# Kernel optimization log

Measured on AMD Instinct MI355X. Metric: run time of the kernel, lower is better.

Reference implementation:

```python
import jax, jax.numpy as jnp
import numpy as np

N_EDGES = 4096
HIDDEN = 256
EDGE_DIM = 128
NUM_HEADS = 4
NUM_GRAPHS = 64


def setup_inputs() -> dict:
    key0 = jax.random.key(0)
    ks = jax.random.split(key0, 10)
    s = 0.02
    inp = {
        "query": jax.random.normal(ks[0], (N_EDGES, HIDDEN), jnp.float32),
        "key": jax.random.normal(ks[1], (N_EDGES, EDGE_DIM), jnp.float32),
        "value": jax.random.normal(ks[2], (N_EDGES, EDGE_DIM), jnp.float32),
        "edge_graph_index": jnp.sort(
            jax.random.randint(ks[3], (N_EDGES,), 0, NUM_GRAPHS)
        ),
        # edge_proj: Linear(edge_context_dim -> hidden_dim)
        "w_edge": jax.random.normal(ks[4], (HIDDEN, EDGE_DIM), jnp.float32) * s,
        "b_edge": jnp.zeros((HIDDEN,), jnp.float32),
        # nn.MultiheadAttention packed in-projection [3H, H] and bias [3H]
        "w_in": jax.random.normal(ks[5], (3 * HIDDEN, HIDDEN), jnp.float32) * s,
        "b_in": jnp.zeros((3 * HIDDEN,), jnp.float32),
        # out_proj: Linear(hidden -> hidden)
        "w_out": jax.random.normal(ks[6], (HIDDEN, HIDDEN), jnp.float32) * s,
        "b_out": jnp.zeros((HIDDEN,), jnp.float32),
    }
    return inp


def reference(query, key, value, edge_graph_index,
              w_edge, b_edge, w_in, b_in, w_out, b_out):
    # Segment-wise cross attention == block-diagonal masked attention over all edges.
    N, H = query.shape
    nh = NUM_HEADS
    dh = H // nh

    # edge feature projection (applied to both key and value, as in the module)
    K = key @ w_edge.T + b_edge      # [N, H]
    V = value @ w_edge.T + b_edge    # [N, H]

    wq, wk, wv = jnp.split(w_in, 3, axis=0)
    bq, bk, bv = jnp.split(b_in, 3)
    Qh = (query @ wq.T + bq).reshape(N, nh, dh)
    Kh = (K @ wk.T + bk).reshape(N, nh, dh)
    Vh = (V @ wv.T + bv).reshape(N, nh, dh)

    scale = 1.0 / jnp.sqrt(jnp.asarray(dh, query.dtype))
    scores = jnp.einsum("nhd,mhd->hnm", Qh, Kh) * scale  # [nh, N, N]

    # attention only within the same graph segment
    same_graph = edge_graph_index[:, None] == edge_graph_index[None, :]  # [N, N]
    neg = jnp.finfo(scores.dtype).min
    scores = jnp.where(same_graph[None, :, :], scores, neg)

    attn = jax.nn.softmax(scores, axis=-1)                 # [nh, N, N]
    out = jnp.einsum("hnm,mhd->nhd", attn, Vh).reshape(N, H)
    out = out @ w_out.T + b_out
    return query + out
```

## Files before the change

kernel.cpp:

```cpp
#include <hip/hip_runtime.h>

#define N_EDGES 4096
#define HIDDEN  256
#define EDGE_DIM 128
#define NUM_HEADS 4
#define NUM_GRAPHS 64
#define DH 64

typedef __attribute__((ext_vector_type(8))) short short8;
typedef __attribute__((ext_vector_type(4))) float f32x4;

__device__ __forceinline__ unsigned short f2bf(float f) {
  unsigned u = __builtin_bit_cast(unsigned, f);
  u += 0x7FFF + ((u >> 16) & 1);
  return (unsigned short)(u >> 16);
}
__device__ __forceinline__ float bf2f(unsigned short u) {
  return __builtin_bit_cast(float, (unsigned)u << 16);
}
__device__ __forceinline__ short8 cvt8(float4 x, float4 y) {
  short8 v;
  v[0] = (short)f2bf(x.x); v[1] = (short)f2bf(x.y);
  v[2] = (short)f2bf(x.z); v[3] = (short)f2bf(x.w);
  v[4] = (short)f2bf(y.x); v[5] = (short)f2bf(y.y);
  v[6] = (short)f2bf(y.z); v[7] = (short)f2bf(y.w);
  return v;
}
__device__ __forceinline__ float4 us4f(ushort4 v) {
  float4 f;
  f.x = bf2f(v.x); f.y = bf2f(v.y); f.z = bf2f(v.z); f.w = bf2f(v.w);
  return f;
}

__device__ __forceinline__ int lbound(const int* __restrict__ a, int n, int v) {
  int lo = 0, hi = n;
  while (lo < hi) { int mid = (lo + hi) >> 1; if (a[mid] < v) lo = mid + 1; else hi = mid; }
  return lo;
}

template<bool ABF, bool WBF, bool OUTF32>
__device__ __forceinline__ void gemm_tile(const void* Ap, const void* Wp,
                                          const float* __restrict__ bias,
                                          const float* __restrict__ res,
                                          void* Cp, const int K,
                                          const int m0, const int n0,
                                          unsigned short* As, unsigned short* Ws) {
  const int t = threadIdx.x;
  const int r = t >> 2, kg = t & 3;
  const int lane = t & 63, w = t >> 6;
  const int quad = lane >> 4, l16 = lane & 15;
  const int wm = (w >> 1) * 32, wn = (w & 1) * 32;
  f32x4 acc[2][2] = {};
  const float*          pa32 = (const float*)Ap          + (size_t)(m0 + r) * K + kg * 16;
  const unsigned short* pa16 = (const unsigned short*)Ap + (size_t)(m0 + r) * K + kg * 16;
  const float*          pw32 = (const float*)Wp          + (size_t)(n0 + r) * K + kg * 16;
  const unsigned short* pw16 = (const unsigned short*)Wp + (size_t)(n0 + r) * K + kg * 16;
  float4 a0, a1, a2, a3, w0, w1, w2, w3;
  short8 a16a, a16b, w16a, w16b;
  if (ABF) { a16a = *(const short8*)pa16; a16b = *(const short8*)(pa16 + 8); }
  else { a0 = *(const float4*)pa32;       a1 = *(const float4*)(pa32 + 4);
         a2 = *(const float4*)(pa32 + 8); a3 = *(const float4*)(pa32 + 12); }
  if (WBF) { w16a = *(const short8*)pw16; w16b = *(const short8*)(pw16 + 8); }
  else { w0 = *(const float4*)pw32;       w1 = *(const float4*)(pw32 + 4);
         w2 = *(const float4*)(pw32 + 8); w3 = *(const float4*)(pw32 + 12); }
  for (int kc = 0; kc < K; kc += 64) {
    short8 na16a, na16b, nw16a, nw16b;
    float4 na0, na1, na2, na3, nw0, nw1, nw2, nw3;
    if (kc + 64 < K) {
      if (ABF) { na16a = *(const short8*)(pa16 + kc + 64);
                 na16b = *(const short8*)(pa16 + kc + 72); }
      else { na0 = *(const float4*)(pa32 + kc + 64); na1 = *(const float4*)(pa32 + kc + 68);
             na2 = *(const float4*)(pa32 + kc + 72); na3 = *(const float4*)(pa32 + kc + 76); }
      if (WBF) { nw16a = *(const short8*)(pw16 + kc + 64);
                 nw16b = *(const short8*)(pw16 + kc + 72); }
      else { nw0 = *(const float4*)(pw32 + kc + 64); nw1 = *(const float4*)(pw32 + kc + 68);
             nw2 = *(const float4*)(pw32 + kc + 72); nw3 = *(const float4*)(pw32 + kc + 76); }
    }
    __syncthreads();
    *(short8*)&As[r * 72 + kg * 16]     = ABF ? a16a : cvt8(a0, a1);
    *(short8*)&As[r * 72 + kg * 16 + 8] = ABF ? a16b : cvt8(a2, a3);
    *(short8*)&Ws[r * 72 + kg * 16]     = WBF ? w16a : cvt8(w0, w1);
    *(short8*)&Ws[r * 72 + kg * 16 + 8] = WBF ? w16b : cvt8(w2, w3);
    __syncthreads();
#pragma unroll
    for (int ks = 0; ks < 2; ++ks) {
      short8 af0 = *(const short8*)&As[(wm + l16) * 72 + ks * 32 + quad * 8];
      short8 af1 = *(const short8*)&As[(wm + 16 + l16) * 72 + ks * 32 + quad * 8];
      short8 bq0 = *(const short8*)&Ws[(wn + l16) * 72 + ks * 32 + quad * 8];
      short8 bq1 = *(const short8*)&Ws[(wn + 16 + l16) * 72 + ks * 32 + quad * 8];
      acc[0][0] = __builtin_amdgcn_mfma_f32_16x16x32_bf16(af0, bq0, acc[0][0], 0, 0, 0);
      acc[0][1] = __builtin_amdgcn_mfma_f32_16x16x32_bf16(af0, bq1, acc[0][1], 0, 0, 0);
      acc[1][0] = __builtin_amdgcn_mfma_f32_16x16x32_bf16(af1, bq0, acc[1][0], 0, 0, 0);
      acc[1][1] = __builtin_amdgcn_mfma_f32_16x16x32_bf16(af1, bq1, acc[1][1], 0, 0, 0);
    }
    a16a = na16a; a16b = na16b; a0 = na0; a1 = na1; a2 = na2; a3 = na3;
    w16a = nw16a; w16b = nw16b; w0 = nw0; w1 = nw1; w2 = nw2; w3 = nw3;
  }
#pragma unroll
  for (int j = 0; j < 2; ++j) {
    const int col = n0 + wn + j * 16 + l16;
    const float bj = bias[col];
#pragma unroll
    for (int i = 0; i < 2; ++i)
#pragma unroll
      for (int reg = 0; reg < 4; ++reg) {
        const int row = m0 + wm + i * 16 + quad * 4 + reg;
        const size_t idx = (size_t)row * HIDDEN + col;
        float v = acc[i][j][reg] + bj;
        if (OUTF32) ((float*)Cp)[idx] = v + res[idx];
        else        ((unsigned short*)Cp)[idx] = f2bf(v);
      }
  }
}

__device__ __forceinline__ void wf_part(int bb, const float* __restrict__ w_in,
                                        const float* __restrict__ b_in,
                                        const float* __restrict__ w_edge,
                                        const float* __restrict__ b_edge,
                                        unsigned short* __restrict__ Wfk,
                                        unsigned short* __restrict__ Wfv,
                                        float* __restrict__ bfk, float* __restrict__ bfv,
                                        unsigned short* As, unsigned short* Bs) {
  const int sel = bb >> 3;
  const int tt  = bb & 7;
  const int n0  = (tt >> 1) * 64;
  const int k0  = (tt & 1) * 64;
  const float* Wp = w_in + (size_t)(256 + 256 * sel) * HIDDEN;
  const float* bp = b_in + 256 + 256 * sel;
  unsigned short* Wf = sel ? Wfv : Wfk;
  float* bf = sel ? bfv : bfk;
  const int t = threadIdx.x;
  const int r = t >> 2, kg = t & 3;
  const int lane = t & 63, w = t >> 6;
  const int quad = lane >> 4, l16 = lane & 15;
  const int wm = (w >> 1) * 32, wn = (w & 1) * 32;
  if (k0 == 0) {
    float s = 0.f;
    const float* wrow = Wp + (size_t)(n0 + r) * HIDDEN + kg * 64;
    const float* be = b_edge + kg * 64;
#pragma unroll
    for (int j = 0; j < 64; j += 4) {
      float4 a = *(const float4*)(wrow + j);
      float4 b = *(const float4*)(be + j);
      s += a.x * b.x + a.y * b.y + a.z * b.z + a.w * b.w;
    }
    s += __shfl_xor(s, 1); s += __shfl_xor(s, 2);
    if (kg == 0) bf[n0 + r] = s + bp[n0 + r];
  }
  f32x4 facc[2][2] = {};
  for (int j0 = 0; j0 < HIDDEN; j0 += 32) {
    __syncthreads();
    { const float* p = Wp + (size_t)(n0 + r) * HIDDEN + j0 + kg * 8;
      float4 x0 = *(const float4*)p, x1 = *(const float4*)(p + 4);
      *(short8*)&As[r * 40 + kg * 8] = cvt8(x0, x1); }
    { const int j = t >> 3, k8 = (t & 7) * 8;
      const float* p = w_edge + (size_t)(j0 + j) * EDGE_DIM + k0 + k8;
      float4 b0 = *(const float4*)p, b1 = *(const float4*)(p + 4);
      float bv[8] = {b0.x, b0.y, b0.z, b0.w, b1.x, b1.y, b1.z, b1.w};
#pragma unroll
      for (int i = 0; i < 8; ++i) Bs[(k8 + i) * 40 + j] = f2bf(bv[i]); }
    __syncthreads();
    short8 af0 = *(const short8*)&As[(wm + l16) * 40 + quad * 8];
    short8 af1 = *(const short8*)&As[(wm + 16 + l16) * 40 + quad * 8];
    short8 bq0 = *(const short8*)&Bs[(wn + l16) * 40 + quad * 8];
    short8 bq1 = *(const short8*)&Bs[(wn + 16 + l16) * 40 + quad * 8];
    facc[0][0] = __builtin_amdgcn_mfma_f32_16x16x32_bf16(af0, bq0, facc[0][0], 0, 0, 0);
    facc[0][1] = __builtin_amdgcn_mfma_f32_16x16x32_bf16(af0, bq1, facc[0][1], 0, 0, 0);
    facc[1][0] = __builtin_amdgcn_mfma_f32_16x16x32_bf16(af1, bq0, facc[1][0], 0, 0, 0);
    facc[1][1] = __builtin_amdgcn_mfma_f32_16x16x32_bf16(af1, bq1, facc[1][1], 0, 0, 0);
  }
#pragma unroll
  for (int jj = 0; jj < 2; ++jj)
#pragma unroll
    for (int ii = 0; ii < 2; ++ii)
#pragma unroll
      for (int reg = 0; reg < 4; ++reg) {
        const int n = wm + ii * 16 + quad * 4 + reg;
        const int k = wn + jj * 16 + l16;
        Wf[(size_t)(n0 + n) * EDGE_DIM + k0 + k] = f2bf(facc[ii][jj][reg]);
      }
}

__global__ __launch_bounds__(256) void k_wf(const float* __restrict__ w_in,
                                            const float* __restrict__ b_in,
                                            const float* __restrict__ w_edge,
                                            const float* __restrict__ b_edge,
                                            const int* __restrict__ gidx,
                                            unsigned short* Wfk, unsigned short* Wfv,
                                            float* bfk, float* bfv, int* segStart) {
  __shared__ unsigned short As[64 * 40];
  __shared__ unsigned short Bs[64 * 40];
  if (blockIdx.x < 16)
    wf_part(blockIdx.x, w_in, b_in, w_edge, b_edge, Wfk, Wfv, bfk, bfv, As, Bs);
  else if (threadIdx.x <= NUM_GRAPHS)
    segStart[threadIdx.x] = lbound(gidx, N_EDGES, threadIdx.x);
}

__global__ __launch_bounds__(256) void k_proj(const float* __restrict__ query,
                                              const float* __restrict__ key,
                                              const float* __restrict__ value,
                                              const float* __restrict__ w_in,
                                              const float* __restrict__ b_in,
                                              const unsigned short* __restrict__ Wfk,
                                              const unsigned short* __restrict__ Wfv,
                                              const float* __restrict__ bfk,
                                              const float* __restrict__ bfv,
                                              unsigned short* Qh, unsigned short* Kh,
                                              unsigned short* Vh) {
  __shared__ unsigned short As[64 * 72];
  __shared__ unsigned short Ws[64 * 72];
  const int m0 = blockIdx.x * 64, n0 = blockIdx.y * 64;
  if (blockIdx.z == 0)
    gemm_tile<false, false, false>(query, w_in, b_in, nullptr, Qh, 256, m0, n0, As, Ws);
  else if (blockIdx.z == 1)
    gemm_tile<false, true, false>(key, Wfk, bfk, nullptr, Kh, 128, m0, n0, As, Ws);
  else
    gemm_tile<false, true, false>(value, Wfv, bfv, nullptr, Vh, 128, m0, n0, As, Ws);
}

__global__ __launch_bounds__(256) void attn_segment(const unsigned short* __restrict__ Qh,
                                                    const unsigned short* __restrict__ Kh,
                                                    const unsigned short* __restrict__ Vh,
                                                    const int* __restrict__ segStart,
                                                    unsigned short* __restrict__ ao) {
  const int graph = blockIdx.x, h = blockIdx.y, zg = blockIdx.z;
  const int segLo = segStart[graph];
  const int segHi = segStart[graph + 1];
  const int segLen = segHi - segLo;
  const int t = threadIdx.x, lane = t & 63, w = t >> 6;
  __shared__ float Qs[16][68], Ks[64][68], Vs[64][68];
  __shared__ float Ps[4][64][4];
  const float scale = 0.125f;
  const int r0 = w * 4;

  for (int chunk = zg; chunk * 16 < segLen; chunk += 8) {
    const int row0 = segLo + chunk * 16;
    const int rows = min(16, segHi - row0);
    __syncthreads();
    { int r = t >> 4, d4 = (t & 15) * 4;
      if (r < rows)
        *(float4*)&Qs[r][d4] =
            us4f(*(const ushort4*)(Qh + (size_t)(row0 + r) * HIDDEN + h * DH + d4)); }

    float accv[4] = {0.f, 0.f, 0.f, 0.f}, lsum[4] = {0.f, 0.f, 0.f, 0.f};

    for (int c0 = segLo; c0 < segHi; c0 += 64) {
      const int tc = min(64, segHi - c0);
      __syncthreads();
#pragma unroll
      for (int it = 0; it < 4; ++it) {
        int s = t + it * 256; int j = s >> 4; int d4 = (s & 15) * 4;
        if (j < tc) {
          *(float4*)&Ks[j][d4] =
              us4f(*(const ushort4*)(Kh + (size_t)(c0 + j) * HIDDEN + h * DH + d4));
          *(float4*)&Vs[j][d4] =
              us4f(*(const ushort4*)(Vh + (size_t)(c0 + j) * HIDDEN + h * DH + d4));
        }
      }
      __syncthreads();
      float4 kreg[16];
#pragma unroll
      for (int d4 = 0; d4 < 16; ++d4) kreg[d4] = *(const float4*)&Ks[lane][d4 * 4];
      float p[4];
#pragma unroll
      for (int r = 0; r < 4; ++r) {
        float s = 0.f;
#pragma unroll
        for (int d4 = 0; d4 < 16; ++d4) {
          float4 q = *(const float4*)&Qs[r0 + r][d4 * 4];
          s += q.x * kreg[d4].x + q.y * kreg[d4].y + q.z * kreg[d4].z + q.w * kreg[d4].w;
        }
        p[r] = (lane < tc && r0 + r < rows) ? __expf(s * scale) : 0.f;
        lsum[r] += p[r];
      }
      float4 p4; p4.x = p[0]; p4.y = p[1]; p4.z = p[2]; p4.w = p[3];
      *(float4*)&Ps[w][lane][0] = p4;
      __asm__ volatile("s_waitcnt lgkmcnt(0)" ::: "memory");
      for (int j = 0; j < tc; ++j) {
        const float v = Vs[j][lane];
        float4 pj = *(const float4*)&Ps[w][j][0];
        accv[0] += pj.x * v; accv[1] += pj.y * v;
        accv[2] += pj.z * v; accv[3] += pj.w * v;
      }
    }
#pragma unroll
    for (int off = 32; off; off >>= 1)
#pragma unroll
      for (int r = 0; r < 4; ++r) lsum[r] += __shfl_xor(lsum[r], off);
#pragma unroll
    for (int r = 0; r < 4; ++r)
      if (r0 + r < rows)
        ao[(size_t)(row0 + r0 + r) * HIDDEN + h * DH + lane] = f2bf(accv[r] / lsum[r]);
  }
}

__global__ __launch_bounds__(256) void k_out(const unsigned short* __restrict__ ao,
                                             const float* __restrict__ w_out,
                                             const float* __restrict__ b_out,
                                             const float* __restrict__ query,
                                             float* __restrict__ out) {
  __shared__ unsigned short As[64 * 72];
  __shared__ unsigned short Ws[64 * 72];
  gemm_tile<true, false, true>(ao, w_out, b_out, query, out, 256,
                               blockIdx.x * 64, blockIdx.y * 64, As, Ws);
}

extern "C" void kernel_launch(void* const* d_in, const int* in_sizes, int n_in,
                              void* d_out, int out_size, void* d_ws, size_t ws_size,
                              hipStream_t stream) {
  const float* query  = (const float*)d_in[0];
  const float* key    = (const float*)d_in[1];
  const float* value  = (const float*)d_in[2];
  const int*   gidx   = (const int*)d_in[3];
  const float* w_edge = (const float*)d_in[4];
  const float* b_edge = (const float*)d_in[5];
  const float* w_in   = (const float*)d_in[6];
  const float* b_in   = (const float*)d_in[7];
  const float* w_out  = (const float*)d_in[8];
  const float* b_out  = (const float*)d_in[9];
  float* out = (float*)d_out;

  int* segStart = (int*)d_ws;
  unsigned short* Qh  = (unsigned short*)((char*)d_ws + 512);
  unsigned short* Kh  = Qh + (size_t)N_EDGES * HIDDEN;
  unsigned short* Vh  = Kh + (size_t)N_EDGES * HIDDEN;
  unsigned short* ao  = Vh + (size_t)N_EDGES * HIDDEN;
  unsigned short* Wfk = ao + (size_t)N_EDGES * HIDDEN;
  unsigned short* Wfv = Wfk + 256 * EDGE_DIM;
  float* bfk = (float*)(Wfv + 256 * EDGE_DIM);
  float* bfv = bfk + 256;

  k_wf<<<dim3(17), 256, 0, stream>>>(w_in, b_in, w_edge, b_edge, gidx,
                                     Wfk, Wfv, bfk, bfv, segStart);
  k_proj<<<dim3(64, 4, 3), 256, 0, stream>>>(query, key, value, w_in, b_in,
                                             Wfk, Wfv, bfk, bfv, Qh, Kh, Vh);
  attn_segment<<<dim3(NUM_GRAPHS, NUM_HEADS, 8), 256, 0, stream>>>(Qh, Kh, Vh,
                                                                   segStart, ao);
  k_out<<<dim3(64, 4), 256, 0, stream>>>(ao, w_out, b_out, query, out);
}
```

Measured before the change: 121.3 us.

## Fuse edge projection and K/V in-projection into single QKV kernel

Removes the separate weight-folding kernel and merges the K/V projection with the edge projection. Each K/V block first computes the edge-projected 64x256 tile into LDS, then multiplies it by the in-projection weights, and Q tiles plus the segment-boundary search run in the same launch. This saves one kernel launch and the dependency between the fold and projection kernels. In exchange, K/V blocks do a two-stage GEMM with more FLOPs per row, use a larger LDS footprint (which may lower occupancy), and get only 128 heavy blocks.

New measurement: 123.9 us. 1.02x slower.

```diff
diff --git a/kernel.cpp b/kernel.cpp
--- a/kernel.cpp
+++ b/kernel.cpp
@@ -113,109 +113,145 @@
   }
 }
 
-__device__ __forceinline__ void wf_part(int bb, const float* __restrict__ w_in,
-                                        const float* __restrict__ b_in,
-                                        const float* __restrict__ w_edge,
-                                        const float* __restrict__ b_edge,
-                                        unsigned short* __restrict__ Wfk,
-                                        unsigned short* __restrict__ Wfv,
-                                        float* __restrict__ bfk, float* __restrict__ bfv,
-                                        unsigned short* As, unsigned short* Bs) {
-  const int sel = bb >> 3;
-  const int tt  = bb & 7;
-  const int n0  = (tt >> 1) * 64;
-  const int k0  = (tt & 1) * 64;
-  const float* Wp = w_in + (size_t)(256 + 256 * sel) * HIDDEN;
-  const float* bp = b_in + 256 + 256 * sel;
-  unsigned short* Wf = sel ? Wfv : Wfk;
-  float* bf = sel ? bfv : bfk;
+union SharedL1 {
+  struct { unsigned short As[64 * 72]; unsigned short Ws[64 * 72]; } g;
+  struct { unsigned short EkS[64 * 264];
+           unsigned short As[64 * 40];
+           unsigned short Ws[256 * 40]; } f;
+};
+
+__device__ __forceinline__ void fused_kv(const float* __restrict__ X,
+                                         const float* __restrict__ w_edge,
+                                         const float* __restrict__ b_edge,
+                                         const float* __restrict__ Wp,
+                                         const float* __restrict__ bp,
+                                         unsigned short* __restrict__ Out,
+                                         const int m0, SharedL1& sh) {
   const int t = threadIdx.x;
   const int r = t >> 2, kg = t & 3;
   const int lane = t & 63, w = t >> 6;
   const int quad = lane >> 4, l16 = lane & 15;
-  const int wm = (w >> 1) * 32, wn = (w & 1) * 32;
-  if (k0 == 0) {
-    float s = 0.f;
-    const float* wrow = Wp + (size_t)(n0 + r) * HIDDEN + kg * 64;
-    const float* be = b_edge + kg * 64;
-#pragma unroll
-    for (int j = 0; j < 64; j += 4) {
-      float4 a = *(const float4*)(wrow + j);
-      float4 b = *(const float4*)(be + j);
-      s += a.x * b.x + a.y * b.y + a.z * b.z + a.w * b.w;
+  unsigned short* EkS = sh.f.EkS;
+  unsigned short* As  = sh.f.As;
+  unsigned short* Ws  = sh.f.Ws;
+  f32x4 acc[4][4] = {};
+
+  const float* px = X + (size_t)(m0 + r) * EDGE_DIM + kg * 8;
+  const float* pw = w_edge + (size_t)t * EDGE_DIM;
+  float4 xa0 = *(const float4*)px, xa1 = *(const float4*)(px + 4);
+  float4 wb[8];
+#pragma unroll
+  for (int i = 0; i < 8; ++i) wb[i] = *(const float4*)(pw + i * 4);
+  for (int kc = 0; kc < EDGE_DIM; kc += 32) {
+    float4 nxa0, nxa1, nwb[8];
+    if (kc + 32 < EDGE_DIM) {
+      nxa0 = *(const float4*)(px + kc + 32); nxa1 = *(const float4*)(px + kc + 36);
+#pragma unroll
+      for (int i = 0; i < 8; ++i) nwb[i] = *(const float4*)(pw + kc + 32 + i * 4);
     }
-    s += __shfl_xor(s, 1); s += __shfl_xor(s, 2);
-    if (kg == 0) bf[n0 + r] = s + bp[n0 + r];
-  }
-  f32x4 facc[2][2] = {};
-  for (int j0 = 0; j0 < HIDDEN; j0 += 32) {
-    __syncthreads();
-    { const float* p = Wp + (size_t)(n0 + r) * HIDDEN + j0 + kg * 8;
-      float4 x0 = *(const float4*)p, x1 = *(const float4*)(p + 4);
-      *(short8*)&As[r * 40 + kg * 8] = cvt8(x0, x1); }
-    { const int j = t >> 3, k8 = (t & 7) * 8;
-      const float* p = w_edge + (size_t)(j0 + j) * EDGE_DIM + k0 + k8;
-      float4 b0 = *(const float4*)p, b1 = *(const float4*)(p + 4);
-      float bv[8] = {b0.x, b0.y, b0.z, b0.w, b1.x, b1.y, b1.z, b1.w};
-#pragma unroll
-      for (int i = 0; i < 8; ++i) Bs[(k8 + i) * 40 + j] = f2bf(bv[i]); }
-    __syncthreads();
-    short8 af0 = *(const short8*)&As[(wm + l16) * 40 + quad * 8];
-    short8 af1 = *(const short8*)&As[(wm + 16 + l16) * 40 + quad * 8];
-    short8 bq0 = *(const short8*)&Bs[(wn + l16) * 40 + quad * 8];
-    short8 bq1 = *(const short8*)&Bs[(wn + 16 + l16) * 40 + quad * 8];
-    facc[0][0] = __builtin_amdgcn_mfma_f32_16x16x32_bf16(af0, bq0, facc[0][0], 0, 0, 0);
-    facc[0][1] = __builtin_amdgcn_mfma_f32_16x16x32_bf16(af0, bq1, facc[0][1], 0, 0, 0);
-    facc[1][0] = __builtin_amdgcn_mfma_f32_16x16x32_bf16(af1, bq0, facc[1][0], 0, 0, 0);
-    facc[1][1] = __builtin_amdgcn_mfma_f32_16x16x32_bf16(af1, bq1, facc[1][1], 0, 0, 0);
-  }
-#pragma unroll
-  for (int jj = 0; jj < 2; ++jj)
-#pragma unroll
-    for (int ii = 0; ii < 2; ++ii)
+    __syncthreads();
+    *(short8*)&As[r * 40 + kg * 8] = cvt8(xa0, xa1);
+#pragma unroll
+    for (int i = 0; i < 4; ++i)
+      *(short8*)&Ws[t * 40 + i * 8] = cvt8(wb[2 * i], wb[2 * i + 1]);
+    __syncthreads();
+    short8 af[4], bf[4];
+#pragma unroll
+    for (int rt = 0; rt < 4; ++rt)
+      af[rt] = *(const short8*)&As[(rt * 16 + l16) * 40 + quad * 8];
+#pragma unroll
+    for (int ct = 0; ct < 4; ++ct)
+      bf[ct] = *(const short8*)&Ws[(w * 64 + ct * 16 + l16) * 40 + quad * 8];
+#pragma unroll
+    for (int rt = 0; rt < 4; ++rt)
+#pragma unroll
+      for (int ct = 0; ct < 4; ++ct)
+        acc[rt][ct] = __builtin_amdgcn_mfma_f32_16x16x32_bf16(af[rt], bf[ct],
+                                                              acc[rt][ct], 0, 0, 0);
+    xa0 = nxa0; xa1 = nxa1;
+#pragma unroll
+    for (int i = 0; i < 8; ++i) wb[i] = nwb[i];
+  }
+#pragma unroll
+  for (int ct = 0; ct < 4; ++ct) {
+    const int col = w * 64 + ct * 16 + l16;
+    const float bj = b_edge[col];
+#pragma unroll
+    for (int rt = 0; rt < 4; ++rt)
 #pragma unroll
       for (int reg = 0; reg < 4; ++reg) {
-        const int n = wm + ii * 16 + quad * 4 + reg;
-        const int k = wn + jj * 16 + l16;
-        Wf[(size_t)(n0 + n) * EDGE_DIM + k0 + k] = f2bf(facc[ii][jj][reg]);
-      }
-}
-
-__global__ __launch_bounds__(256) void k_wf(const float* __restrict__ w_in,
-                                            const float* __restrict__ b_in,
-                                            const float* __restrict__ w_edge,
-                                            const float* __restrict__ b_edge,
-                                            const int* __restrict__ gidx,
-                                            unsigned short* Wfk, unsigned short* Wfv,
-                                            float* bfk, float* bfv, int* segStart) {
-  __shared__ unsigned short As[64 * 40];
-  __shared__ unsigned short Bs[64 * 40];
-  if (blockIdx.x < 16)
-    wf_part(blockIdx.x, w_in, b_in, w_edge, b_edge, Wfk, Wfv, bfk, bfv, As, Bs);
-  else if (threadIdx.x <= NUM_GRAPHS)
+        EkS[(rt * 16 + quad * 4 + reg) * 264 + col] = f2bf(acc[rt][ct][reg] + bj);
+        acc[rt][ct][reg] = 0.f;
+      }
+  }
+
+  const float* pw2 = Wp + (size_t)t * HIDDEN;
+#pragma unroll
+  for (int i = 0; i < 8; ++i) wb[i] = *(const float4*)(pw2 + i * 4);
+  for (int kc = 0; kc < HIDDEN; kc += 32) {
+    float4 nwb[8];
+    if (kc + 32 < HIDDEN)
+#pragma unroll
+      for (int i = 0; i < 8; ++i) nwb[i] = *(const float4*)(pw2 + kc + 32 + i * 4);
+    __syncthreads();
+#pragma unroll
+    for (int i = 0; i < 4; ++i)
+      *(short8*)&Ws[t * 40 + i * 8] = cvt8(wb[2 * i], wb[2 * i + 1]);
+    __syncthreads();
+    short8 af[4], bf[4];
+#pragma unroll
+    for (int rt = 0; rt < 4; ++rt)
+      af[rt] = *(const short8*)&EkS[(rt * 16 + l16) * 264 + kc + quad * 8];
+#pragma unroll
+    for (int ct = 0; ct < 4; ++ct)
+      bf[ct] = *(const short8*)&Ws[(w * 64 + ct * 16 + l16) * 40 + quad * 8];
+#pragma unroll
+    for (int rt = 0; rt < 4; ++rt)
+#pragma unroll
+      for (int ct = 0; ct < 4; ++ct)
+        acc[rt][ct] = __builtin_amdgcn_mfma_f32_16x16x32_bf16(af[rt], bf[ct],
+                                                              acc[rt][ct], 0, 0, 0);
+#pragma unroll
+    for (int i = 0; i < 8; ++i) wb[i] = nwb[i];
+  }
+#pragma unroll
+  for (int ct = 0; ct < 4; ++ct) {
+    const int col = w * 64 + ct * 16 + l16;
+    const float bj = bp[col];
+#pragma unroll
+    for (int rt = 0; rt < 4; ++rt)
+#pragma unroll
+      for (int reg = 0; reg < 4; ++reg)
+        Out[(size_t)(m0 + rt * 16 + quad * 4 + reg) * HIDDEN + col] =
+            f2bf(acc[rt][ct][reg] + bj);
+  }
+}
+
+__global__ __launch_bounds__(256) void k_qkv(const float* __restrict__ query,
+                                             const float* __restrict__ key,
+                                             const float* __restrict__ value,
+                                             const float* __restrict__ w_in,
+                                             const float* __restrict__ b_in,
+                                             const float* __restrict__ w_edge,
+                                             const float* __restrict__ b_edge,
+                                             const int* __restrict__ gidx,
+                                             unsigned short* Qh, unsigned short* Kh,
+                                             unsigned short* Vh, int* segStart) {
+  __shared__ SharedL1 sh;
+  const int b = blockIdx.x;
+  if (b < 64) {
+    fused_kv(key, w_edge, b_edge, w_in + (size_t)256 * HIDDEN, b_in + 256,
+             Kh, b * 64, sh);
+  } else if (b < 128) {
+    fused_kv(value, w_edge, b_edge, w_in + (size_t)512 * HIDDEN, b_in + 512,
+             Vh, (b - 64) * 64, sh);
+  } else if (b < 384) {
+    const int q = b - 128;
+    gemm_tile<false, false, false>(query, w_in, b_in, nullptr, Qh, 256,
+                                   (q & 63) * 64, (q >> 6) * 64, sh.g.As, sh.g.Ws);
+  } else if (threadIdx.x <= NUM_GRAPHS) {
     segStart[threadIdx.x] = lbound(gidx, N_EDGES, threadIdx.x);
-}
-
-__global__ __launch_bounds__(256) void k_proj(const float* __restrict__ query,
-                                              const float* __restrict__ key,
-                                              const float* __restrict__ value,
-                                              const float* __restrict__ w_in,
-                                              const float* __restrict__ b_in,
-                                              const unsigned short* __restrict__ Wfk,
-                                              const unsigned short* __restrict__ Wfv,
-                                              const float* __restrict__ bfk,
-                                              const float* __restrict__ bfv,
-                                              unsigned short* Qh, unsigned short* Kh,
-                                              unsigned short* Vh) {
-  __shared__ unsigned short As[64 * 72];
-  __shared__ unsigned short Ws[64 * 72];
-  const int m0 = blockIdx.x * 64, n0 = blockIdx.y * 64;
-  if (blockIdx.z == 0)
-    gemm_tile<false, false, false>(query, w_in, b_in, nullptr, Qh, 256, m0, n0, As, Ws);
-  else if (blockIdx.z == 1)
-    gemm_tile<false, true, false>(key, Wfk, bfk, nullptr, Kh, 128, m0, n0, As, Ws);
-  else
-    gemm_tile<false, true, false>(value, Wfv, bfv, nullptr, Vh, 128, m0, n0, As, Ws);
+  }
 }
 
 __global__ __launch_bounds__(256) void attn_segment(const unsigned short* __restrict__ Qh,
@@ -321,19 +357,13 @@
   float* out = (float*)d_out;
 
   int* segStart = (int*)d_ws;
-  unsigned short* Qh  = (unsigned short*)((char*)d_ws + 512);
-  unsigned short* Kh  = Qh + (size_t)N_EDGES * HIDDEN;
-  unsigned short* Vh  = Kh + (size_t)N_EDGES * HIDDEN;
-  unsigned short* ao  = Vh + (size_t)N_EDGES * HIDDEN;
-  unsigned short* Wfk = ao + (size_t)N_EDGES * HIDDEN;
-  unsigned short* Wfv = Wfk + 256 * EDGE_DIM;
-  float* bfk = (float*)(Wfv + 256 * EDGE_DIM);
-  float* bfv = bfk + 256;
-
-  k_wf<<<dim3(17), 256, 0, stream>>>(w_in, b_in, w_edge, b_edge, gidx,
-                                     Wfk, Wfv, bfk, bfv, segStart);
-  k_proj<<<dim3(64, 4, 3), 256, 0, stream>>>(query, key, value, w_in, b_in,
-                                             Wfk, Wfv, bfk, bfv, Qh, Kh, Vh);
+  unsigned short* Qh = (unsigned short*)((char*)d_ws + 512);
+  unsigned short* Kh = Qh + (size_t)N_EDGES * HIDDEN;
+  unsigned short* Vh = Kh + (size_t)N_EDGES * HIDDEN;
+  unsigned short* ao = Vh + (size_t)N_EDGES * HIDDEN;
+
+  k_qkv<<<dim3(385), 256, 0, stream>>>(query, key, value, w_in, b_in,
+                                       w_edge, b_edge, gidx, Qh, Kh, Vh, segStart);
   attn_segment<<<dim3(NUM_GRAPHS, NUM_HEADS, 8), 256, 0, stream>>>(Qh, Kh, Vh,
                                                                    segStart, ao);
   k_out<<<dim3(64, 4), 256, 0, stream>>>(ao, w_out, b_out, query, out);
```

## Overlap Q projection with fused-weight precompute by regrouping kernel launches

Applied to the files above, without the earlier changes.

The Q projection, which does not depend on the fused edge/in-proj weights, is moved into the first kernel alongside the Wf precompute and segment-start search. The second kernel now only computes K and V. Previously a tiny 17-block kernel ran by itself, leaving most CUs idle. Now that work shares a launch with the 256 Q tiles, using a union of shared memory layouts. The cost is a slightly larger shared allocation per block and uneven block work within the first launch.

New measurement: 120.6 us. About the same (-0.6%).

```diff
diff --git a/kernel.cpp b/kernel.cpp
--- a/kernel.cpp
+++ b/kernel.cpp
@@ -181,38 +181,43 @@
       }
 }
 
-__global__ __launch_bounds__(256) void k_wf(const float* __restrict__ w_in,
-                                            const float* __restrict__ b_in,
-                                            const float* __restrict__ w_edge,
-                                            const float* __restrict__ b_edge,
-                                            const int* __restrict__ gidx,
-                                            unsigned short* Wfk, unsigned short* Wfv,
-                                            float* bfk, float* bfv, int* segStart) {
-  __shared__ unsigned short As[64 * 40];
-  __shared__ unsigned short Bs[64 * 40];
-  if (blockIdx.x < 16)
-    wf_part(blockIdx.x, w_in, b_in, w_edge, b_edge, Wfk, Wfv, bfk, bfv, As, Bs);
-  else if (threadIdx.x <= NUM_GRAPHS)
-    segStart[threadIdx.x] = lbound(gidx, N_EDGES, threadIdx.x);
-}
-
-__global__ __launch_bounds__(256) void k_proj(const float* __restrict__ query,
-                                              const float* __restrict__ key,
-                                              const float* __restrict__ value,
+union SharedL1 {
+  struct { unsigned short As[64 * 72]; unsigned short Ws[64 * 72]; } g;
+  struct { unsigned short As[64 * 40]; unsigned short Bs[64 * 40]; } w;
+};
+
+__global__ __launch_bounds__(256) void k_q_wf(const float* __restrict__ query,
                                               const float* __restrict__ w_in,
                                               const float* __restrict__ b_in,
-                                              const unsigned short* __restrict__ Wfk,
-                                              const unsigned short* __restrict__ Wfv,
-                                              const float* __restrict__ bfk,
-                                              const float* __restrict__ bfv,
-                                              unsigned short* Qh, unsigned short* Kh,
-                                              unsigned short* Vh) {
+                                              const float* __restrict__ w_edge,
+                                              const float* __restrict__ b_edge,
+                                              const int* __restrict__ gidx,
+                                              unsigned short* Qh,
+                                              unsigned short* Wfk, unsigned short* Wfv,
+                                              float* bfk, float* bfv, int* segStart) {
+  __shared__ SharedL1 sh;
+  const int b = blockIdx.x;
+  if (b < 256) {
+    gemm_tile<false, false, false>(query, w_in, b_in, nullptr, Qh, 256,
+                                   (b & 63) * 64, (b >> 6) * 64, sh.g.As, sh.g.Ws);
+  } else if (b < 272) {
+    wf_part(b - 256, w_in, b_in, w_edge, b_edge, Wfk, Wfv, bfk, bfv, sh.w.As, sh.w.Bs);
+  } else if (threadIdx.x <= NUM_GRAPHS) {
+    segStart[threadIdx.x] = lbound(gidx, N_EDGES, threadIdx.x);
+  }
+}
+
+__global__ __launch_bounds__(256) void k_kv(const float* __restrict__ key,
+                                            const float* __restrict__ value,
+                                            const unsigned short* __restrict__ Wfk,
+                                            const unsigned short* __restrict__ Wfv,
+                                            const float* __restrict__ bfk,
+                                            const float* __restrict__ bfv,
+                                            unsigned short* Kh, unsigned short* Vh) {
   __shared__ unsigned short As[64 * 72];
   __shared__ unsigned short Ws[64 * 72];
   const int m0 = blockIdx.x * 64, n0 = blockIdx.y * 64;
   if (blockIdx.z == 0)
-    gemm_tile<false, false, false>(query, w_in, b_in, nullptr, Qh, 256, m0, n0, As, Ws);
-  else if (blockIdx.z == 1)
     gemm_tile<false, true, false>(key, Wfk, bfk, nullptr, Kh, 128, m0, n0, As, Ws);
   else
     gemm_tile<false, true, false>(value, Wfv, bfv, nullptr, Vh, 128, m0, n0, As, Ws);
@@ -330,10 +335,9 @@
   float* bfk = (float*)(Wfv + 256 * EDGE_DIM);
   float* bfv = bfk + 256;
 
-  k_wf<<<dim3(17), 256, 0, stream>>>(w_in, b_in, w_edge, b_edge, gidx,
-                                     Wfk, Wfv, bfk, bfv, segStart);
-  k_proj<<<dim3(64, 4, 3), 256, 0, stream>>>(query, key, value, w_in, b_in,
-                                             Wfk, Wfv, bfk, bfv, Qh, Kh, Vh);
+  k_q_wf<<<dim3(273), 256, 0, stream>>>(query, w_in, b_in, w_edge, b_edge, gidx,
+                                        Qh, Wfk, Wfv, bfk, bfv, segStart);
+  k_kv<<<dim3(64, 4, 2), 256, 0, stream>>>(key, value, Wfk, Wfv, bfk, bfv, Kh, Vh);
   attn_segment<<<dim3(NUM_GRAPHS, NUM_HEADS, 8), 256, 0, stream>>>(Qh, Kh, Vh,
                                                                    segStart, ao);
   k_out<<<dim3(64, 4), 256, 0, stream>>>(ao, w_out, b_out, query, out);
```
